# Kernel optimization log

Measured on AMD Instinct MI355X. Metric: run time of the kernel, lower is better.

## Reference

```python
import jax, jax.numpy as jnp
import numpy as np

N_NODES = 100000


def gcn_conv(x, src, dst, W, b, n):
    # PyG GCNConv: add self-loops, symmetric deg^-1/2 normalization,
    # linear transform, gather->scatter-add aggregation, + bias.
    loop = jnp.arange(n, dtype=src.dtype)
    s = jnp.concatenate([src, loop])
    d = jnp.concatenate([dst, loop])
    deg = jax.ops.segment_sum(jnp.ones_like(d, dtype=x.dtype), d, num_segments=n)
    dinv = jnp.where(deg > 0, jax.lax.rsqrt(deg), jnp.zeros_like(deg))
    norm = dinv[s] * dinv[d]            # [E+N]
    h = x @ W                            # [N, out] (transform before propagate)
    msg = h[s] * norm[:, None]           # gather + scale
    out = jax.ops.segment_sum(msg, d, num_segments=n)  # scatter-add to dst
    return out + b


def setup_inputs() -> dict:
    key = jax.random.key(0)
    k = jax.random.split(key, 6)
    n, e, c_in, hid, c_out = N_NODES, 2500000, 5, 32, 1
    x = jax.random.normal(k[0], (n, c_in), dtype=jnp.float32)
    edge_index = jax.random.randint(k[1], (2, e), 0, n, dtype=jnp.int64)
    # Glorot-style init for GCN weights, zero bias (PyG default)
    W1 = jax.random.normal(k[2], (c_in, hid), dtype=jnp.float32) * (1.0 / np.sqrt(c_in))
    b1 = jnp.zeros((hid,), dtype=jnp.float32)
    W2 = jax.random.normal(k[3], (hid, c_out), dtype=jnp.float32) * (1.0 / np.sqrt(hid))
    b2 = jnp.zeros((c_out,), dtype=jnp.float32)
    return {"x": x, "edge_index": edge_index, "W1": W1, "b1": b1, "W2": W2, "b2": b2}


def reference(x, edge_index, W1, b1, W2, b2):
    n = x.shape[0]
    src, dst = edge_index[0], edge_index[1]
    h = jax.nn.relu(gcn_conv(x, src, dst, W1, b1, n))
    # dropout p=0.3 is identity at inference (training=False)
    return jax.nn.sigmoid(gcn_conv(h, src, dst, W2, b2, n))
```

## Files before the change

### kernel.cpp

```cpp
#include <hip/hip_runtime.h>
#include <hip/hip_cooperative_groups.h>
#include <math.h>

namespace cg = cooperative_groups;


#define NB_SHIFT  8
#define BNODES    256
#define NBK       512
#define CAP       8192
#define CAP_SHIFT 13
#define CHUNK     4888
#define PBLK      512
#define GRID      512

struct SMemP0 {
    int sp[CHUNK];
    unsigned short sb[CHUNK];
    int cnt[NBK], ofs[NBK], cur[NBK], gbase[NBK];
};
struct SMemP1 {
    int stage2[CAP];
    int ofs[BNODES], cnt[BNODES], cur[BNODES];
    float w1[160], bb1[32], w2[32];
};
union SMem { SMemP0 p0; SMemP1 p1; };

__global__ __launch_bounds__(PBLK, 4) void k_fused(
        const int* __restrict__ src, const int* __restrict__ dst, int E,
        const float* __restrict__ x,
        const float* __restrict__ W1, const float* __restrict__ b1,
        const float* __restrict__ W2, const float* __restrict__ b2,
        float* __restrict__ out,
        int* __restrict__ pairs, int* __restrict__ bcur,
        float* __restrict__ h2s, float* __restrict__ xs, int n, int nb) {
    __shared__ SMem sm;
    cg::grid_group grid = cg::this_grid();
    const int tid = threadIdx.x;
    const int blk = blockIdx.x;
    const int nbase = blk << NB_SHIFT;

    {
        int base = blk * CHUNK;
        if (base < E) {
            int m = min(CHUNK, E - base);
            sm.p0.cnt[tid] = 0;
            __syncthreads();
            for (int i = tid; i < m; i += 2 * PBLK) {
                int i1 = i + PBLK;
                int k0 = dst[base + i] >> NB_SHIFT;
                int k1 = (i1 < m) ? (dst[base + i1] >> NB_SHIFT) : -1;
                atomicAdd(&sm.p0.cnt[k0], 1);
                if (k1 >= 0) atomicAdd(&sm.p0.cnt[k1], 1);
            }
            __syncthreads();
            int v = sm.p0.cnt[tid];
            sm.p0.ofs[tid] = v;
            __syncthreads();
            for (int off = 1; off < NBK; off <<= 1) {
                int u = (tid >= off) ? sm.p0.ofs[tid - off] : 0;
                __syncthreads();
                sm.p0.ofs[tid] += u;
                __syncthreads();
            }
            int pre = sm.p0.ofs[tid] - v;
            sm.p0.ofs[tid] = pre;
            sm.p0.cur[tid] = pre;
            sm.p0.gbase[tid] = (tid << CAP_SHIFT)
                             + (v ? atomicAdd(&bcur[tid], v) : 0);
            __syncthreads();
            for (int i = tid; i < m; i += 4 * PBLK) {
                int ia = i + PBLK, ib = i + 2 * PBLK, ic = i + 3 * PBLK;
                int s0 = src[base + i], d0 = dst[base + i];
                int s1 = 0, d1 = 0, s2 = 0, d2 = 0, s3 = 0, d3 = 0;
                if (ia < m) { s1 = src[base + ia]; d1 = dst[base + ia]; }
                if (ib < m) { s2 = src[base + ib]; d2 = dst[base + ib]; }
                if (ic < m) { s3 = src[base + ic]; d3 = dst[base + ic]; }
                int b0 = d0 >> NB_SHIFT;
                int p0 = atomicAdd(&sm.p0.cur[b0], 1);
                sm.p0.sp[p0] = ((d0 & (BNODES - 1)) << 24) | s0;
                sm.p0.sb[p0] = (unsigned short)b0;
                if (ia < m) {
                    int b1k = d1 >> NB_SHIFT;
                    int p1 = atomicAdd(&sm.p0.cur[b1k], 1);
                    sm.p0.sp[p1] = ((d1 & (BNODES - 1)) << 24) | s1;
                    sm.p0.sb[p1] = (unsigned short)b1k;
                }
                if (ib < m) {
                    int b2k = d2 >> NB_SHIFT;
                    int p2 = atomicAdd(&sm.p0.cur[b2k], 1);
                    sm.p0.sp[p2] = ((d2 & (BNODES - 1)) << 24) | s2;
                    sm.p0.sb[p2] = (unsigned short)b2k;
                }
                if (ic < m) {
                    int b3k = d3 >> NB_SHIFT;
                    int p3 = atomicAdd(&sm.p0.cur[b3k], 1);
                    sm.p0.sp[p3] = ((d3 & (BNODES - 1)) << 24) | s3;
                    sm.p0.sb[p3] = (unsigned short)b3k;
                }
            }
            __syncthreads();
            for (int i = tid; i < m; i += PBLK) {
                int b = sm.p0.sb[i];
                pairs[sm.p0.gbase[b] + (i - sm.p0.ofs[b])] = sm.p0.sp[i];
            }
        }
    }
    grid.sync();

    if (blk < nb) {
        int base = blk << CAP_SHIFT;
        int len = min(bcur[blk], CAP);
        if (tid < 160) sm.p1.w1[tid] = W1[tid];
        else if (tid < 192) sm.p1.bb1[tid - 160] = b1[tid - 160];
        else if (tid < 224) sm.p1.w2[tid - 192] = W2[tid - 192];
        if (tid < BNODES) sm.p1.cnt[tid] = 0;
        __syncthreads();
        for (int i = tid; i < len; i += PBLK)
            atomicAdd(&sm.p1.cnt[((unsigned)pairs[base + i]) >> 24], 1);
        __syncthreads();
        int v = (tid < BNODES) ? sm.p1.cnt[tid] : 0;
        if (tid < BNODES) sm.p1.ofs[tid] = v;
        __syncthreads();
        for (int off = 1; off < BNODES; off <<= 1) {
            int u = (tid < BNODES && tid >= off) ? sm.p1.ofs[tid - off] : 0;
            __syncthreads();
            if (tid < BNODES) sm.p1.ofs[tid] += u;
            __syncthreads();
        }
        if (tid < BNODES) {
            int pre = sm.p1.ofs[tid] - v;
            sm.p1.ofs[tid] = pre;
            sm.p1.cur[tid] = pre;
            int node = nbase + tid;
            if (node < n) {
                float di = rsqrtf((float)v + 1.0f);
                const float* xr = x + (size_t)node * 5;
                float* xo = xs + ((size_t)node << 3);
#pragma unroll
                for (int k = 0; k < 5; ++k) xo[k] = xr[k] * di;
            }
        }
        __syncthreads();
        for (int i = tid; i < len; i += 4 * PBLK) {
            int ia = i + PBLK, ib = i + 2 * PBLK, ic = i + 3 * PBLK;
            int v0 = pairs[base + i];
            int v1 = (ia < len) ? pairs[base + ia] : -1;
            int v2 = (ib < len) ? pairs[base + ib] : -1;
            int v3 = (ic < len) ? pairs[base + ic] : -1;
            int p0 = atomicAdd(&sm.p1.cur[((unsigned)v0) >> 24], 1);
            sm.p1.stage2[p0] = v0 & 0x00FFFFFF;
            if (v1 != -1) {
                int p1 = atomicAdd(&sm.p1.cur[((unsigned)v1) >> 24], 1);
                sm.p1.stage2[p1] = v1 & 0x00FFFFFF;
            }
            if (v2 != -1) {
                int p2 = atomicAdd(&sm.p1.cur[((unsigned)v2) >> 24], 1);
                sm.p1.stage2[p2] = v2 & 0x00FFFFFF;
            }
            if (v3 != -1) {
                int p3 = atomicAdd(&sm.p1.cur[((unsigned)v3) >> 24], 1);
                sm.p1.stage2[p3] = v3 & 0x00FFFFFF;
            }
        }
    }
    grid.sync();

    if (blk < nb) {
        int t2 = tid >> 1, half = tid & 1;
        int node = nbase + t2;
        if (node < n) {
            int beg = sm.p1.ofs[t2], dg = sm.p1.cnt[t2];
            float a0 = 0.f, a1 = 0.f, a2 = 0.f, a3 = 0.f, a4 = 0.f;
            if (!half) {
                const float* xo = xs + ((size_t)node << 3);
                a0 = xo[0]; a1 = xo[1]; a2 = xo[2]; a3 = xo[3]; a4 = xo[4];
            }
            for (int e = beg + half; e < beg + dg; e += 2) {
                int s = sm.p1.stage2[e];
                const float* xr = xs + ((size_t)s << 3);
                float4 q = *(const float4*)xr;
                float q4 = xr[4];
                a0 += q.x; a1 += q.y; a2 += q.z; a3 += q.w; a4 += q4;
            }
            a0 += __shfl_xor(a0, 1); a1 += __shfl_xor(a1, 1);
            a2 += __shfl_xor(a2, 1); a3 += __shfl_xor(a3, 1);
            a4 += __shfl_xor(a4, 1);
            if (!half) {
                float di = rsqrtf((float)dg + 1.0f);
                a0 *= di; a1 *= di; a2 *= di; a3 *= di; a4 *= di;
                float sum = 0.f;
#pragma unroll
                for (int c = 0; c < 32; ++c) {
                    float z = sm.p1.bb1[c] + a0 * sm.p1.w1[c]
                            + a1 * sm.p1.w1[32 + c] + a2 * sm.p1.w1[64 + c]
                            + a3 * sm.p1.w1[96 + c] + a4 * sm.p1.w1[128 + c];
                    sum += fmaxf(z, 0.f) * sm.p1.w2[c];
                }
                h2s[node] = sum * di;
            }
        }
    }
    grid.sync();

    if (blk < nb) {
        int t2 = tid >> 1, half = tid & 1;
        int node = nbase + t2;
        if (node >= n) return;
        int beg = sm.p1.ofs[t2], dg = sm.p1.cnt[t2];
        float a = 0.f;
        for (int e = beg + half; e < beg + dg; e += 2)
            a += h2s[sm.p1.stage2[e]];
        a += __shfl_xor(a, 1);
        if (!half) {
            float di = rsqrtf((float)dg + 1.0f);
            float vv = di * (a + h2s[node]) + b2[0];
            out[node] = 1.0f / (1.0f + __expf(-vv));
        }
    }
}


__global__ __launch_bounds__(512) void k_part(const int* __restrict__ src,
                                              const int* __restrict__ dst, int E,
                                              int* __restrict__ bcur,
                                              int* __restrict__ pairs) {
    __shared__ int sp[CHUNK];
    __shared__ unsigned short sb[CHUNK];
    __shared__ int cnt[NBK], ofs[NBK], cur[NBK], gbase[NBK];
    int tid = threadIdx.x;
    int base = blockIdx.x * CHUNK;
    int m = min(CHUNK, E - base);

    if (tid < NBK) cnt[tid] = 0;
    __syncthreads();
    for (int i = tid; i < m; i += 2 * 512) {
        int i1 = i + 512;
        int k0 = dst[base + i] >> NB_SHIFT;
        int k1 = (i1 < m) ? (dst[base + i1] >> NB_SHIFT) : -1;
        atomicAdd(&cnt[k0], 1);
        if (k1 >= 0) atomicAdd(&cnt[k1], 1);
    }
    __syncthreads();
    int v = cnt[tid];
    ofs[tid] = v;
    __syncthreads();
    for (int off = 1; off < NBK; off <<= 1) {
        int u = (tid >= off) ? ofs[tid - off] : 0;
        __syncthreads();
        ofs[tid] += u;
        __syncthreads();
    }
    int pre = ofs[tid] - v;
    ofs[tid] = pre;
    cur[tid] = pre;
    gbase[tid] = (tid << CAP_SHIFT) + (v ? atomicAdd(&bcur[tid], v) : 0);
    __syncthreads();
    for (int i = tid; i < m; i += 4 * 512) {
        int ia = i + 512, ib = i + 1024, ic = i + 1536;
        int s0 = src[base + i], d0 = dst[base + i];
        int s1 = 0, d1 = 0, s2 = 0, d2 = 0, s3 = 0, d3 = 0;
        if (ia < m) { s1 = src[base + ia]; d1 = dst[base + ia]; }
        if (ib < m) { s2 = src[base + ib]; d2 = dst[base + ib]; }
        if (ic < m) { s3 = src[base + ic]; d3 = dst[base + ic]; }
        int b0 = d0 >> NB_SHIFT;
        int p0 = atomicAdd(&cur[b0], 1);
        sp[p0] = ((d0 & (BNODES - 1)) << 24) | s0;
        sb[p0] = (unsigned short)b0;
        if (ia < m) {
            int b1 = d1 >> NB_SHIFT;
            int p1 = atomicAdd(&cur[b1], 1);
            sp[p1] = ((d1 & (BNODES - 1)) << 24) | s1;
            sb[p1] = (unsigned short)b1;
        }
        if (ib < m) {
            int b2 = d2 >> NB_SHIFT;
            int p2 = atomicAdd(&cur[b2], 1);
            sp[p2] = ((d2 & (BNODES - 1)) << 24) | s2;
            sb[p2] = (unsigned short)b2;
        }
        if (ic < m) {
            int b3 = d3 >> NB_SHIFT;
            int p3 = atomicAdd(&cur[b3], 1);
            sp[p3] = ((d3 & (BNODES - 1)) << 24) | s3;
            sb[p3] = (unsigned short)b3;
        }
    }
    __syncthreads();
    for (int i = tid; i < m; i += 512) {
        int b = sb[i];
        pairs[gbase[b] + (i - ofs[b])] = sp[i];
    }
}

__global__ __launch_bounds__(512) void k_sorta(const int* __restrict__ pairs,
                                               const int* __restrict__ bcur,
                                               const float* __restrict__ x,
                                               float* __restrict__ dinv,
                                               float* __restrict__ xs,
                                               int* __restrict__ nofs,
                                               int* __restrict__ deg, int n) {
    __shared__ int cnt[BNODES], scn[BNODES];
    int tid = threadIdx.x;
    int b = blockIdx.x;
    int base = b << CAP_SHIFT;
    int len = min(bcur[b], CAP);

    if (tid < BNODES) cnt[tid] = 0;
    __syncthreads();
    for (int i = tid; i < len; i += 512)
        atomicAdd(&cnt[((unsigned)pairs[base + i]) >> 24], 1);
    __syncthreads();
    int v = (tid < BNODES) ? cnt[tid] : 0;
    if (tid < BNODES) scn[tid] = v;
    __syncthreads();
    for (int off = 1; off < BNODES; off <<= 1) {
        int u = (tid < BNODES && tid >= off) ? scn[tid - off] : 0;
        __syncthreads();
        if (tid < BNODES) scn[tid] += u;
        __syncthreads();
    }
    if (tid < BNODES) {
        int node = (b << NB_SHIFT) + tid;
        if (node < n) {
            nofs[node] = base + scn[tid] - v;
            deg[node] = v;
            float di = rsqrtf((float)v + 1.0f);
            dinv[node] = di;
            const float* xr = x + (size_t)node * 5;
            float* xo = xs + ((size_t)node << 3);
#pragma unroll
            for (int k = 0; k < 5; ++k) xo[k] = xr[k] * di;
        }
    }
}

__global__ __launch_bounds__(512) void k_sortagg1(int* __restrict__ pairs,
                                                  const int* __restrict__ bcur,
                                                  const int* __restrict__ nofs,
                                                  const int* __restrict__ deg,
                                                  const float* __restrict__ xs,
                                                  const float* __restrict__ dinv,
                                                  const float* __restrict__ W1,
                                                  const float* __restrict__ b1,
                                                  const float* __restrict__ W2,
                                                  float* __restrict__ h2s, int n) {
    __shared__ int stage2[CAP];
    __shared__ int ofs[BNODES], cnt[BNODES], cur[BNODES];
    __shared__ float w1[160], bb1[32], w2[32];
    int tid = threadIdx.x;
    int b = blockIdx.x;
    int nbase = b << NB_SHIFT;
    int base = b << CAP_SHIFT;
    int len = min(bcur[b], CAP);

    if (tid < 160) w1[tid] = W1[tid];
    else if (tid < 192) bb1[tid - 160] = b1[tid - 160];
    else if (tid < 224) w2[tid - 192] = W2[tid - 192];
    if (tid < BNODES) {
        int node = nbase + tid;
        int o = 0, c = 0;
        if (node < n) { o = nofs[node] - base; c = deg[node]; }
        ofs[tid] = o; cnt[tid] = c; cur[tid] = o;
    }
    __syncthreads();
    for (int i = tid; i < len; i += 2048) {
        int ia = i + 512, ib = i + 1024, ic = i + 1536;
        int v0 = pairs[base + i];
        int v1 = (ia < len) ? pairs[base + ia] : -1;
        int v2 = (ib < len) ? pairs[base + ib] : -1;
        int v3 = (ic < len) ? pairs[base + ic] : -1;
        int p0 = atomicAdd(&cur[((unsigned)v0) >> 24], 1);
        stage2[p0] = v0 & 0x00FFFFFF;
        if (v1 != -1) {
            int p1 = atomicAdd(&cur[((unsigned)v1) >> 24], 1);
            stage2[p1] = v1 & 0x00FFFFFF;
        }
        if (v2 != -1) {
            int p2 = atomicAdd(&cur[((unsigned)v2) >> 24], 1);
            stage2[p2] = v2 & 0x00FFFFFF;
        }
        if (v3 != -1) {
            int p3 = atomicAdd(&cur[((unsigned)v3) >> 24], 1);
            stage2[p3] = v3 & 0x00FFFFFF;
        }
    }
    __syncthreads();
    {
        int len4 = len >> 2;
        const int4* s4 = (const int4*)stage2;
        int4* p4 = (int4*)(pairs + base);
        for (int i = tid; i < len4; i += 512) p4[i] = s4[i];
        for (int i = (len4 << 2) + tid; i < len; i += 512)
            pairs[base + i] = stage2[i];
    }
    int t2 = tid >> 1, half = tid & 1;
    int node = nbase + t2;
    if (node >= n) return;
    int beg = ofs[t2], dg = cnt[t2];
    float a0 = 0.f, a1 = 0.f, a2 = 0.f, a3 = 0.f, a4 = 0.f;
    if (!half) {
        const float* xo = xs + ((size_t)node << 3);
        a0 = xo[0]; a1 = xo[1]; a2 = xo[2]; a3 = xo[3]; a4 = xo[4];
    }
    for (int e = beg + half; e < beg + dg; e += 2) {
        int s = stage2[e];
        const float* xr = xs + ((size_t)s << 3);
        float4 q = *(const float4*)xr;
        float q4 = xr[4];
        a0 += q.x; a1 += q.y; a2 += q.z; a3 += q.w; a4 += q4;
    }
    a0 += __shfl_xor(a0, 1); a1 += __shfl_xor(a1, 1); a2 += __shfl_xor(a2, 1);
    a3 += __shfl_xor(a3, 1); a4 += __shfl_xor(a4, 1);
    if (half) return;
    float di = dinv[node];
    a0 *= di; a1 *= di; a2 *= di; a3 *= di; a4 *= di;
    float sum = 0.f;
#pragma unroll
    for (int c = 0; c < 32; ++c) {
        float z = bb1[c] + a0 * w1[c] + a1 * w1[32 + c] + a2 * w1[64 + c]
                         + a3 * w1[96 + c] + a4 * w1[128 + c];
        sum += fmaxf(z, 0.f) * w2[c];
    }
    h2s[node] = sum * di;
}

__global__ __launch_bounds__(256) void k_agg2(const int* __restrict__ pairs,
                                              const int* __restrict__ nofs,
                                              const int* __restrict__ deg,
                                              const float* __restrict__ h2s,
                                              const float* __restrict__ dinv,
                                              const float* __restrict__ b2,
                                              float* __restrict__ out, int n) {
    int tid = threadIdx.x;
    int node = blockIdx.x * 64 + (tid >> 2);
    int q = tid & 3;
    if (node >= n) return;
    int beg = nofs[node], dg = deg[node];
    float a = 0.f;
    for (int e = beg + q; e < beg + dg; e += 4) a += h2s[pairs[e]];
    a += __shfl_xor(a, 1);
    a += __shfl_xor(a, 2);
    if (q) return;
    float v = dinv[node] * (a + h2s[node]) + b2[0];
    out[node] = 1.0f / (1.0f + __expf(-v));
}

extern "C" void kernel_launch(void* const* d_in, const int* in_sizes, int n_in,
                              void* d_out, int out_size, void* d_ws, size_t ws_size,
                              hipStream_t stream) {
    const float* x  = (const float*)d_in[0];
    const int*   ei = (const int*)d_in[1];
    const float* W1 = (const float*)d_in[2];
    const float* b1 = (const float*)d_in[3];
    const float* W2 = (const float*)d_in[4];
    const float* b2 = (const float*)d_in[5];
    float* out = (float*)d_out;

    const int n = in_sizes[0] / 5;
    const int E = in_sizes[1] / 2;
    const int* src = ei;
    const int* dst = ei + E;
    const int nb = (n + BNODES - 1) >> NB_SHIFT;

    int* wsi = (int*)d_ws;
    int*   pairs = wsi;
    int*   bcur  = wsi + ((size_t)(nb + 1) << CAP_SHIFT);
    int*   deg   = bcur + NBK;
    int*   nofs  = deg + n;
    float* dinv  = (float*)(nofs + n);
    float* h2s   = dinv + n;
    float* xs    = h2s + n;

    const int nchunk = (E + CHUNK - 1) / CHUNK;
    const int g = nchunk > nb ? nchunk : nb;

    static int use_coop = -1;
    if (use_coop < 0) {
        int dev = 0, ncu = 0, maxb = 0;
        hipGetDevice(&dev);
        hipDeviceGetAttribute(&ncu, hipDeviceAttributeMultiprocessorCount, dev);
        hipError_t e = hipOccupancyMaxActiveBlocksPerMultiprocessor(
                &maxb, k_fused, PBLK, 0);
        int coop = 0;
        hipDeviceGetAttribute(&coop, hipDeviceAttributeCooperativeLaunch, dev);
        use_coop = (e == hipSuccess && coop && (long)maxb * ncu >= g) ? 1 : 0;
    }

    hipMemsetAsync(bcur, 0, NBK * sizeof(int), stream);

    if (use_coop) {
        void* args[] = {(void*)&src, (void*)&dst, (void*)&E, (void*)&x,
                        (void*)&W1, (void*)&b1, (void*)&W2, (void*)&b2,
                        (void*)&out, (void*)&pairs, (void*)&bcur,
                        (void*)&h2s, (void*)&xs, (void*)&n, (void*)&nb};
        hipError_t e = hipLaunchCooperativeKernel((const void*)k_fused,
                                                  dim3(g), dim3(PBLK),
                                                  args, 0, stream);
        if (e == hipSuccess) return;
        use_coop = 0;
    }

    const int nagg = (n + 63) / 64;
    k_part<<<nchunk, 512, 0, stream>>>(src, dst, E, bcur, pairs);
    k_sorta<<<nb, 512, 0, stream>>>(pairs, bcur, x, dinv, xs, nofs, deg, n);
    k_sortagg1<<<nb, 512, 0, stream>>>(pairs, bcur, nofs, deg, xs, dinv,
                                       W1, b1, W2, h2s, n);
    k_agg2<<<nagg, 256, 0, stream>>>(pairs, nofs, deg, h2s, dinv, b2, out, n);
}
```

Measured before the change: 141.8 us.

## Replace cooperative grid syncs with split arrive/wait barriers and register-held records

Swaps cg grid.sync for a custom atomic-counter global barrier split into arrive and wait, so independent work (loading weights, x rows, the local scatter into stage2) overlaps the barrier latency. Shared-memory Hillis-Steele scans become wave shuffle scans. Each thread keeps its pair records in registers (up to 16) so pairs is read once instead of twice. This adds register pressure and relies on the barrier counter being zeroed by memset before every launch.

```diff
diff --git a/kernel.cpp b/kernel.cpp
--- a/kernel.cpp
+++ b/kernel.cpp
@@ -1,8 +1,5 @@
 #include <hip/hip_runtime.h>
-#include <hip/hip_cooperative_groups.h>
 #include <math.h>
-
-namespace cg = cooperative_groups;
 
 
 #define NB_SHIFT  8
@@ -12,19 +9,39 @@
 #define CAP_SHIFT 13
 #define CHUNK     4888
 #define PBLK      512
-#define GRID      512
+#define RPT       16
 
 struct SMemP0 {
     int sp[CHUNK];
     unsigned short sb[CHUNK];
     int cnt[NBK], ofs[NBK], cur[NBK], gbase[NBK];
+    int wtmp[8];
 };
 struct SMemP1 {
     int stage2[CAP];
     int ofs[BNODES], cnt[BNODES], cur[BNODES];
     float w1[160], bb1[32], w2[32];
+    int wtmp[8];
 };
 union SMem { SMemP0 p0; SMemP1 p1; };
+
+__device__ __forceinline__ void gbar_arrive(int* bar, int tid) {
+    __syncthreads();
+    if (tid == 0) {
+        __threadfence();
+        __hip_atomic_fetch_add(bar, 1, __ATOMIC_RELAXED,
+                               __HIP_MEMORY_SCOPE_AGENT);
+    }
+}
+__device__ __forceinline__ void gbar_wait(int* bar, int tgt, int tid) {
+    if (tid == 0) {
+        while (__hip_atomic_load(bar, __ATOMIC_RELAXED,
+                                 __HIP_MEMORY_SCOPE_AGENT) < tgt)
+            __builtin_amdgcn_s_sleep(1);
+        __threadfence();
+    }
+    __syncthreads();
+}
 
 __global__ __launch_bounds__(PBLK, 4) void k_fused(
         const int* __restrict__ src, const int* __restrict__ dst, int E,
@@ -32,12 +49,13 @@
         const float* __restrict__ W1, const float* __restrict__ b1,
         const float* __restrict__ W2, const float* __restrict__ b2,
         float* __restrict__ out,
-        int* __restrict__ pairs, int* __restrict__ bcur,
+        int* __restrict__ pairs, int* __restrict__ bcur, int* __restrict__ gbar,
         float* __restrict__ h2s, float* __restrict__ xs, int n, int nb) {
     __shared__ SMem sm;
-    cg::grid_group grid = cg::this_grid();
-    const int tid = threadIdx.x;
-    const int blk = blockIdx.x;
+    const int tid  = threadIdx.x;
+    const int blk  = blockIdx.x;
+    const int G    = gridDim.x;
+    const int lane = tid & 63, wv = tid >> 6;
     const int nbase = blk << NB_SHIFT;
 
     {
@@ -55,15 +73,25 @@
             }
             __syncthreads();
             int v = sm.p0.cnt[tid];
-            sm.p0.ofs[tid] = v;
+            int s = v;
+#pragma unroll
+            for (int d = 1; d < 64; d <<= 1) {
+                int t = __shfl_up(s, d);
+                if (lane >= d) s += t;
+            }
+            if (lane == 63) sm.p0.wtmp[wv] = s;
             __syncthreads();
-            for (int off = 1; off < NBK; off <<= 1) {
-                int u = (tid >= off) ? sm.p0.ofs[tid - off] : 0;
-                __syncthreads();
-                sm.p0.ofs[tid] += u;
-                __syncthreads();
-            }
-            int pre = sm.p0.ofs[tid] - v;
+            if (wv == 0) {
+                int t = (lane < 8) ? sm.p0.wtmp[lane] : 0;
+#pragma unroll
+                for (int d = 1; d < 8; d <<= 1) {
+                    int u = __shfl_up(t, d);
+                    if (lane >= d) t += u;
+                }
+                if (lane < 8) sm.p0.wtmp[lane] = t;
+            }
+            __syncthreads();
+            int pre = s + (wv ? sm.p0.wtmp[wv - 1] : 0) - v;
             sm.p0.ofs[tid] = pre;
             sm.p0.cur[tid] = pre;
             sm.p0.gbase[tid] = (tid << CAP_SHIFT)
@@ -106,65 +134,79 @@
             }
         }
     }
-    grid.sync();
-
+    gbar_arrive(gbar, tid);
+    float xr0 = 0.f, xr1 = 0.f, xr2 = 0.f, xr3 = 0.f, xr4 = 0.f;
     if (blk < nb) {
-        int base = blk << CAP_SHIFT;
-        int len = min(bcur[blk], CAP);
         if (tid < 160) sm.p1.w1[tid] = W1[tid];
         else if (tid < 192) sm.p1.bb1[tid - 160] = b1[tid - 160];
         else if (tid < 224) sm.p1.w2[tid - 192] = W2[tid - 192];
-        if (tid < BNODES) sm.p1.cnt[tid] = 0;
-        __syncthreads();
-        for (int i = tid; i < len; i += PBLK)
-            atomicAdd(&sm.p1.cnt[((unsigned)pairs[base + i]) >> 24], 1);
+        if (tid < BNODES) {
+            sm.p1.cnt[tid] = 0;
+            int node = nbase + tid;
+            if (node < n) {
+                const float* xp = x + (size_t)node * 5;
+                xr0 = xp[0]; xr1 = xp[1]; xr2 = xp[2]; xr3 = xp[3]; xr4 = xp[4];
+            }
+        }
+    }
+    gbar_wait(gbar, G, tid);
+
+    int nrec = 0;
+    int rec[RPT];
+    if (blk < nb) {
+        int base = blk << CAP_SHIFT;
+        int len = min(((volatile int*)bcur)[blk], CAP);
+#pragma unroll
+        for (int j = 0; j < RPT; ++j) {
+            int i = tid + j * PBLK;
+            if (i < len) { rec[j] = pairs[base + i]; nrec = j + 1; }
+        }
+#pragma unroll
+        for (int j = 0; j < RPT; ++j)
+            if (j < nrec) atomicAdd(&sm.p1.cnt[((unsigned)rec[j]) >> 24], 1);
         __syncthreads();
         int v = (tid < BNODES) ? sm.p1.cnt[tid] : 0;
-        if (tid < BNODES) sm.p1.ofs[tid] = v;
-        __syncthreads();
-        for (int off = 1; off < BNODES; off <<= 1) {
-            int u = (tid < BNODES && tid >= off) ? sm.p1.ofs[tid - off] : 0;
-            __syncthreads();
-            if (tid < BNODES) sm.p1.ofs[tid] += u;
-            __syncthreads();
-        }
+        int s = v;
+#pragma unroll
+        for (int d = 1; d < 64; d <<= 1) {
+            int t = __shfl_up(s, d);
+            if (lane >= d) s += t;
+        }
+        if (lane == 63 && wv < 4) sm.p1.wtmp[wv] = s;
+        __syncthreads();
+        if (wv == 0) {
+            int t = (lane < 4) ? sm.p1.wtmp[lane] : 0;
+#pragma unroll
+            for (int d = 1; d < 4; d <<= 1) {
+                int u = __shfl_up(t, d);
+                if (lane >= d) t += u;
+            }
+            if (lane < 4) sm.p1.wtmp[lane] = t;
+        }
+        __syncthreads();
         if (tid < BNODES) {
-            int pre = sm.p1.ofs[tid] - v;
+            int pre = s + (wv ? sm.p1.wtmp[wv - 1] : 0) - v;
             sm.p1.ofs[tid] = pre;
             sm.p1.cur[tid] = pre;
             int node = nbase + tid;
             if (node < n) {
                 float di = rsqrtf((float)v + 1.0f);
-                const float* xr = x + (size_t)node * 5;
                 float* xo = xs + ((size_t)node << 3);
-#pragma unroll
-                for (int k = 0; k < 5; ++k) xo[k] = xr[k] * di;
-            }
-        }
-        __syncthreads();
-        for (int i = tid; i < len; i += 4 * PBLK) {
-            int ia = i + PBLK, ib = i + 2 * PBLK, ic = i + 3 * PBLK;
-            int v0 = pairs[base + i];
-            int v1 = (ia < len) ? pairs[base + ia] : -1;
-            int v2 = (ib < len) ? pairs[base + ib] : -1;
-            int v3 = (ic < len) ? pairs[base + ic] : -1;
-            int p0 = atomicAdd(&sm.p1.cur[((unsigned)v0) >> 24], 1);
-            sm.p1.stage2[p0] = v0 & 0x00FFFFFF;
-            if (v1 != -1) {
-                int p1 = atomicAdd(&sm.p1.cur[((unsigned)v1) >> 24], 1);
-                sm.p1.stage2[p1] = v1 & 0x00FFFFFF;
-            }
-            if (v2 != -1) {
-                int p2 = atomicAdd(&sm.p1.cur[((unsigned)v2) >> 24], 1);
-                sm.p1.stage2[p2] = v2 & 0x00FFFFFF;
-            }
-            if (v3 != -1) {
-                int p3 = atomicAdd(&sm.p1.cur[((unsigned)v3) >> 24], 1);
-                sm.p1.stage2[p3] = v3 & 0x00FFFFFF;
-            }
-        }
-    }
-    grid.sync();
+                xo[0] = xr0 * di; xo[1] = xr1 * di; xo[2] = xr2 * di;
+                xo[3] = xr3 * di; xo[4] = xr4 * di;
+            }
+        }
+    }
+    gbar_arrive(gbar, tid);
+    if (blk < nb) {
+#pragma unroll
+        for (int j = 0; j < RPT; ++j)
+            if (j < nrec) {
+                int p = atomicAdd(&sm.p1.cur[((unsigned)rec[j]) >> 24], 1);
+                sm.p1.stage2[p] = rec[j] & 0x00FFFFFF;
+            }
+    }
+    gbar_wait(gbar, 2 * G, tid);
 
     if (blk < nb) {
         int t2 = tid >> 1, half = tid & 1;
@@ -177,8 +219,8 @@
                 a0 = xo[0]; a1 = xo[1]; a2 = xo[2]; a3 = xo[3]; a4 = xo[4];
             }
             for (int e = beg + half; e < beg + dg; e += 2) {
-                int s = sm.p1.stage2[e];
-                const float* xr = xs + ((size_t)s << 3);
+                int sidx = sm.p1.stage2[e];
+                const float* xr = xs + ((size_t)sidx << 3);
                 float4 q = *(const float4*)xr;
                 float q4 = xr[4];
                 a0 += q.x; a1 += q.y; a2 += q.z; a3 += q.w; a4 += q4;
@@ -201,7 +243,8 @@
             }
         }
     }
-    grid.sync();
+    gbar_arrive(gbar, tid);
+    gbar_wait(gbar, 3 * G, tid);
 
     if (blk < nb) {
         int t2 = tid >> 1, half = tid & 1;
@@ -466,7 +509,8 @@
     int* wsi = (int*)d_ws;
     int*   pairs = wsi;
     int*   bcur  = wsi + ((size_t)(nb + 1) << CAP_SHIFT);
-    int*   deg   = bcur + NBK;
+    int*   gbar  = bcur + NBK;
+    int*   deg   = gbar + 16;
     int*   nofs  = deg + n;
     float* dinv  = (float*)(nofs + n);
     float* h2s   = dinv + n;
@@ -487,12 +531,12 @@
         use_coop = (e == hipSuccess && coop && (long)maxb * ncu >= g) ? 1 : 0;
     }
 
-    hipMemsetAsync(bcur, 0, NBK * sizeof(int), stream);
+    hipMemsetAsync(bcur, 0, (NBK + 16) * sizeof(int), stream);
 
     if (use_coop) {
         void* args[] = {(void*)&src, (void*)&dst, (void*)&E, (void*)&x,
                         (void*)&W1, (void*)&b1, (void*)&W2, (void*)&b2,
-                        (void*)&out, (void*)&pairs, (void*)&bcur,
+                        (void*)&out, (void*)&pairs, (void*)&bcur, (void*)&gbar,
                         (void*)&h2s, (void*)&xs, (void*)&n, (void*)&nb};
         hipError_t e = hipLaunchCooperativeKernel((const void*)k_fused,
                                                   dim3(g), dim3(PBLK),
```

New measurement: 143.7 us. About the same (+1.4%).
